# Kernel optimization log

Hardware: AMD Instinct MI355X
Metric: run time of the kernel (lower is better)

The kernel has to match this reference:

```python
import jax, jax.numpy as jnp
import numpy as np

N, E = 50000, 800000
DIM_IN, DIM_H, DIM_OUT, HEADS = 128, 32, 16, 4
HID = DIM_H * HEADS  # 128
FINAL = DIM_OUT * HEADS  # 64
NEG_SLOPE = 0.2


def _glorot(key, shape):
    fan_in, fan_out = shape[0], shape[-1] if len(shape) > 1 else shape[0]
    lim = jnp.sqrt(6.0 / (fan_in + fan_out)).astype(jnp.float32)
    return jax.random.uniform(key, shape, jnp.float32, -lim, lim)


def setup_inputs() -> dict:
    key = jax.random.key(0)
    ks = jax.random.split(key, 16)
    x = jax.random.normal(ks[0], (N, DIM_IN), jnp.float32)
    edge_index = jax.random.randint(ks[1], (2, E), 0, N, dtype=jnp.int64)
    inp = {"x": x, "edge_index": edge_index}
    # layer 1: DIM_IN -> HEADS*DIM_H
    inp["Wl1"] = _glorot(ks[2], (DIM_IN, HEADS * DIM_H))
    inp["Wr1"] = _glorot(ks[3], (DIM_IN, HEADS * DIM_H))
    inp["att1"] = _glorot(ks[4], (HEADS, DIM_H))
    inp["b1"] = jnp.zeros((HEADS * DIM_H,), jnp.float32)
    # layer 2: HID -> HEADS*DIM_H
    inp["Wl2"] = _glorot(ks[5], (HID, HEADS * DIM_H))
    inp["Wr2"] = _glorot(ks[6], (HID, HEADS * DIM_H))
    inp["att2"] = _glorot(ks[7], (HEADS, DIM_H))
    inp["b2"] = jnp.zeros((HEADS * DIM_H,), jnp.float32)
    # layer 3: HID -> HEADS*DIM_OUT
    inp["Wl3"] = _glorot(ks[8], (HID, HEADS * DIM_OUT))
    inp["Wr3"] = _glorot(ks[9], (HID, HEADS * DIM_OUT))
    inp["att3"] = _glorot(ks[10], (HEADS, DIM_OUT))
    inp["b3"] = jnp.zeros((HEADS * DIM_OUT,), jnp.float32)
    return inp


def gatv2_conv(x, src, dst, Wl, Wr, att, b, heads, ch):
    n = x.shape[0]
    xl = (x @ Wl).reshape(n, heads, ch)  # source-side transform
    xr = (x @ Wr).reshape(n, heads, ch)  # target-side transform
    m = xl[src] + xr[dst]                 # [E, H, C]
    e = jnp.einsum('ehc,hc->eh', jax.nn.leaky_relu(m, NEG_SLOPE), att)
    # segment softmax over incoming edges of each dst node
    emax = jax.ops.segment_max(e, dst, num_segments=n)
    ex = jnp.exp(e - emax[dst])
    denom = jax.ops.segment_sum(ex, dst, num_segments=n)
    alpha = ex / denom[dst]               # [E, H]
    out = jax.ops.segment_sum(alpha[:, :, None] * xl[src], dst, num_segments=n)
    return out.reshape(n, heads * ch) + b


def reference(x, edge_index, Wl1, Wr1, att1, b1, Wl2, Wr2, att2, b2, Wl3, Wr3, att3, b3):
    n = x.shape[0]
    loops = jnp.arange(n, dtype=edge_index.dtype)
    src = jnp.concatenate([edge_index[0], loops])  # PyG add_self_loops=True
    dst = jnp.concatenate([edge_index[1], loops])
    # dropout is identity in eval mode
    h = jax.nn.elu(gatv2_conv(x, src, dst, Wl1, Wr1, att1, b1, HEADS, DIM_H))
    h = jax.nn.elu(gatv2_conv(h, src, dst, Wl2, Wr2, att2, b2, HEADS, DIM_H))
    h = gatv2_conv(h, src, dst, Wl3, Wr3, att3, b3, HEADS, DIM_OUT)
    return jax.nn.log_softmax(h, axis=1)
```

## Files before the change

### kernel.cpp

```cpp
#include <hip/hip_runtime.h>
#include <math.h>

constexpr int DIN  = 128;
constexpr int FSH  = 10;
constexpr int NFBM = 64;
constexpr int LCAP = 160;
constexpr int RND  = 4096;
constexpr int FCAP = 18432;

typedef __attribute__((ext_vector_type(8))) short short8;
typedef __attribute__((ext_vector_type(4))) float f32x4;
typedef __attribute__((ext_vector_type(2))) float f32x2;

__device__ __forceinline__ unsigned short f2bf(float f) {
  unsigned u = __float_as_uint(f);
  u = (u + 0x7FFF + ((u >> 16) & 1)) >> 16;
  return (unsigned short)u;
}
__device__ __forceinline__ float bflo(unsigned u) { return __uint_as_float(u << 16); }
__device__ __forceinline__ float bfhi(unsigned u) { return __uint_as_float(u & 0xFFFF0000u); }
__device__ __forceinline__ f32x2 bfpair(unsigned u) {
  f32x2 r; r.x = bflo(u); r.y = bfhi(u); return r;
}
__device__ __forceinline__ f32x2 fabs2(f32x2 v) {
  f32x2 r; r.x = fabsf(v.x); r.y = fabsf(v.y); return r;
}

typedef const __attribute__((address_space(1))) unsigned int guint_t;
typedef __attribute__((address_space(3))) unsigned int luint_t;
__device__ __forceinline__ void async16(const void* g, void* l) {
  __builtin_amdgcn_global_load_lds((guint_t*)g, (luint_t*)l, 16, 0, 0);
}

__device__ __forceinline__ float score8(uint4 u, const f32x2* xrp,
                                        const f32x2* a6, const f32x2* a4, f32x2* xp) {
  xp[0] = bfpair(u.x); xp[1] = bfpair(u.y);
  xp[2] = bfpair(u.z); xp[3] = bfpair(u.w);
  f32x2 acc = {0.f, 0.f};
#pragma unroll
  for (int j = 0; j < 4; ++j) {
    f32x2 t = xp[j] + xrp[j];
    acc += t * a6[j] + fabs2(t) * a4[j];
  }
  float p = acc.x + acc.y;
  p += __shfl_xor(p, 1, 64);
  p += __shfl_xor(p, 2, 64);
  return p;
}

__device__ __forceinline__ float score4(uint2 u, const f32x2* xrp,
                                        const f32x2* a6, const f32x2* a4, f32x2* xp) {
  xp[0] = bfpair(u.x); xp[1] = bfpair(u.y);
  f32x2 acc = {0.f, 0.f};
#pragma unroll
  for (int j = 0; j < 2; ++j) {
    f32x2 t = xp[j] + xrp[j];
    acc += t * a6[j] + fabs2(t) * a4[j];
  }
  float p = acc.x + acc.y;
  p += __shfl_xor(p, 1, 64);
  p += __shfl_xor(p, 2, 64);
  return p;
}


__global__ __launch_bounds__(256) void bucket_append_kernel(const int* __restrict__ ei,
    int* __restrict__ gcnt, unsigned* __restrict__ gpairs, int E, int nfb) {
  __shared__ unsigned buf[NFBM * LCAP];
  __shared__ int cnt[NFBM];
  __shared__ int gbase[NFBM];
  const int tid = threadIdx.x;
  if (tid < NFBM) cnt[tid] = 0;
  __syncthreads();

  const int k0 = blockIdx.x * RND;
  for (int i = tid; i < RND; i += 256) {
    int k = k0 + i;
    if (k >= E) break;
    int src = ei[k], dst = ei[E + k];
    int fb = dst >> FSH;
    int pos = atomicAdd(&cnt[fb], 1);
    if (pos < LCAP)
      buf[fb * LCAP + pos] = (unsigned)src | ((unsigned)(dst & ((1 << FSH) - 1)) << 16);
  }
  __syncthreads();

  if (tid < nfb) gbase[tid] = atomicAdd(&gcnt[tid], min(cnt[tid], LCAP));
  __syncthreads();

  const int wid = tid >> 6, lane = tid & 63;
  for (int fb = wid; fb < nfb; fb += 4) {
    int c  = min(cnt[fb], LCAP);
    int gb = gbase[fb];
    if (gb >= FCAP) continue;
    c = min(c, FCAP - gb);
    unsigned* dstp = gpairs + (size_t)fb * FCAP + gb;
    const unsigned* srcp = &buf[fb * LCAP];
    for (int i = lane; i < c; i += 64) dstp[i] = srcp[i];
  }
}

__global__ __launch_bounds__(256) void bucket_build_kernel(const unsigned* __restrict__ gpairs,
    const int* __restrict__ gcnt, int* __restrict__ row_ptr,
    unsigned short* __restrict__ edge_src, int n, int nfb) {
  const int b   = blockIdx.x;
  const int tid = threadIdx.x;
  const int lane = tid & 63, wid = tid >> 6;
  __shared__ int hist[1024];
  __shared__ int wsum[4];
  __shared__ int base_s;

  const int d0 = b << FSH;
  const int nvalid = min(1 << FSH, n - d0);

  if (wid == 0) {
    int term = 0;
    if (lane < b)
      term = min(gcnt[lane], FCAP) + min(1 << FSH, n - (lane << FSH));
#pragma unroll
    for (int o = 32; o >= 1; o >>= 1) term += __shfl_xor(term, o, 64);
    if (lane == 0) base_s = term;
  }
  for (int i = tid; i < 1024; i += 256) hist[i] = (i < nvalid) ? 1 : 0;
  __syncthreads();

  const int cnt = min(gcnt[b], FCAP);
  const unsigned* bp = gpairs + (size_t)b * FCAP;
  for (int i = tid; i < cnt; i += 256)
    atomicAdd(&hist[bp[i] >> 16], 1);
  __syncthreads();

  const int i4 = tid * 4;
  int h0 = hist[i4], h1 = hist[i4 + 1], h2 = hist[i4 + 2], h3 = hist[i4 + 3];
  int s = h0 + h1 + h2 + h3;
  int incl = s;
#pragma unroll
  for (int o = 1; o < 64; o <<= 1) {
    int t = __shfl_up(incl, o, 64);
    if (lane >= o) incl += t;
  }
  if (lane == 63) wsum[wid] = incl;
  __syncthreads();
  int wo = 0;
  for (int wq = 0; wq < wid; ++wq) wo += wsum[wq];
  const int base = base_s;
  int ex[4];
  ex[0] = wo + incl - s;
  ex[1] = ex[0] + h0;
  ex[2] = ex[1] + h1;
  ex[3] = ex[2] + h2;
#pragma unroll
  for (int j = 0; j < 4; ++j) {
    int d = i4 + j;
    if (d < nvalid) {
      row_ptr[d0 + d] = base + ex[j];
      edge_src[base + ex[j]] = (unsigned short)(d0 + d);
      hist[d] = ex[j] + 1;
    } else if (d0 + d == n) {
      row_ptr[n] = base + ex[j];
    }
  }
  if (b == nfb - 1 && d0 + 1024 <= n && tid == 0) row_ptr[n] = base + cnt + nvalid;
  __syncthreads();

  for (int i = tid; i < cnt; i += 256) {
    unsigned p = bp[i];
    int pos = atomicAdd(&hist[p >> 16], 1);
    edge_src[base + pos] = (unsigned short)(p & 0xFFFFu);
  }
}

__global__ __launch_bounds__(256) void cvt_w_kernel(
    const float* __restrict__ Wl1, const float* __restrict__ Wr1,
    const float* __restrict__ Wl2, const float* __restrict__ Wr2,
    const float* __restrict__ Wl3, const float* __restrict__ Wr3,
    unsigned short* __restrict__ Wt, int* __restrict__ gcnt) {
  if (blockIdx.x == 0 && threadIdx.x < NFBM) gcnt[threadIdx.x] = 0;
  int e = blockIdx.x * 256 + threadIdx.x;
  if (e >= 81920) return;
  const float* src; int N; int off;
  if (e < 65536) {
    int m = e >> 14; off = e & 16383; N = 128;
    src = (m == 0) ? Wl1 : (m == 1) ? Wr1 : (m == 2) ? Wl2 : Wr2;
  } else {
    int e2 = e - 65536; int m = e2 >> 13; off = e2 & 8191; N = 64;
    src = m ? Wr3 : Wl3;
  }
  int nn = off >> 7, k = off & 127;
  Wt[e] = f2bf(src[(size_t)k * N + nn]);
}


template<int NC, bool CVT>
__global__ __launch_bounds__(256) void gemm2_mfma(const void* __restrict__ Ap,
    const unsigned short* __restrict__ Wlt, const unsigned short* __restrict__ Wrt,
    unsigned short* __restrict__ outl, unsigned short* __restrict__ outr, int M) {
  constexpr int WNB = NC / 16;
  __shared__ char lds[16384 + NC * 256];
  char* As = lds;
  char* Ws = lds + 16384;
  const int tid  = threadIdx.x;
  const int w    = tid >> 6, lane = tid & 63;
  const int q    = lane >> 4, r15 = lane & 15;
  const int row0 = blockIdx.x * 64;

  if constexpr (CVT) {
    const float* Af = (const float*)Ap;
    for (int idx = tid * 4; idx < 64 * 128; idx += 1024) {
      int rl = idx >> 7, k = idx & 127;
      int rg = row0 + rl; if (rg >= M) rg = M - 1;
      float4 v = *(const float4*)&Af[(size_t)rg * 128 + k];
      uint2 pk;
      pk.x = (unsigned)f2bf(v.x) | ((unsigned)f2bf(v.y) << 16);
      pk.y = (unsigned)f2bf(v.z) | ((unsigned)f2bf(v.w) << 16);
      char* addr = As + (rl >> 4) * 4096 + (k >> 5) * 1024 +
                   ((((k >> 3) & 3) * 16) + (rl & 15)) * 16 + (k & 7) * 2;
      *(uint2*)addr = pk;
    }
  } else {
    const unsigned short* A = (const unsigned short*)Ap;
    int r = row0 + w * 16 + r15; if (r >= M) r = M - 1;
    const char* g = (const char*)A + (size_t)r * 256 + q * 16;
    char* l = As + w * 4096;
#pragma unroll
    for (int kk = 0; kk < 4; ++kk) async16(g + kk * 64, l + kk * 1024);
  }
  for (int nt = w; nt < WNB; nt += 4) {
    const char* g = (const char*)Wlt + ((size_t)(nt * 16 + r15)) * 256 + q * 16;
    char* l = Ws + nt * 4096;
#pragma unroll
    for (int kk = 0; kk < 4; ++kk) async16(g + kk * 64, l + kk * 1024);
  }
  __syncthreads();

  const char* aw = As + w * 4096;
  f32x4 acc[WNB] = {};
#pragma unroll
  for (int kk = 0; kk < 4; ++kk) {
    short8 af = *(const short8*)(aw + kk * 1024 + (size_t)lane * 16);
#pragma unroll
    for (int nt = 0; nt < WNB; ++nt) {
      short8 bf = *(const short8*)(Ws + (nt * 4 + kk) * 1024 + (size_t)lane * 16);
      acc[nt] = __builtin_amdgcn_mfma_f32_16x16x32_bf16(af, bf, acc[nt], 0, 0, 0);
    }
  }
  {
    int rowb = row0 + w * 16 + q * 4;
#pragma unroll
    for (int nt = 0; nt < WNB; ++nt)
#pragma unroll
      for (int r = 0; r < 4; ++r) {
        int rr = rowb + r;
        if (rr < M) outl[(size_t)rr * NC + nt * 16 + r15] = f2bf(acc[nt][r]);
      }
  }
  __syncthreads();
  for (int nt = w; nt < WNB; nt += 4) {
    const char* g = (const char*)Wrt + ((size_t)(nt * 16 + r15)) * 256 + q * 16;
    char* l = Ws + nt * 4096;
#pragma unroll
    for (int kk = 0; kk < 4; ++kk) async16(g + kk * 64, l + kk * 1024);
  }
  __syncthreads();

  f32x4 acc2[WNB] = {};
#pragma unroll
  for (int kk = 0; kk < 4; ++kk) {
    short8 af = *(const short8*)(aw + kk * 1024 + (size_t)lane * 16);
#pragma unroll
    for (int nt = 0; nt < WNB; ++nt) {
      short8 bf = *(const short8*)(Ws + (nt * 4 + kk) * 1024 + (size_t)lane * 16);
      acc2[nt] = __builtin_amdgcn_mfma_f32_16x16x32_bf16(af, bf, acc2[nt], 0, 0, 0);
    }
  }
  {
    int rowb = row0 + w * 16 + q * 4;
#pragma unroll
    for (int nt = 0; nt < WNB; ++nt)
#pragma unroll
      for (int r = 0; r < 4; ++r) {
        int rr = rowb + r;
        if (rr < M) outr[(size_t)rr * NC + nt * 16 + r15] = f2bf(acc2[nt][r]);
      }
  }
}


__global__ __launch_bounds__(256) void aggregate128_kernel(
    const unsigned short* __restrict__ xl, const unsigned short* __restrict__ xr,
    const float* __restrict__ att, const float* __restrict__ bias,
    const int* __restrict__ row_ptr, const unsigned short* __restrict__ edge_src,
    unsigned short* __restrict__ out, int n) {
  const int tid  = threadIdx.x;
  const int r    = tid & 15;
  const int node = blockIdx.x * 16 + (tid >> 4);
  if (node >= n) return;
  const int c0 = r * 8;

  f32x2 xrp[4];
  {
    uint4 u = *(const uint4*)&xr[(size_t)node * 128 + c0];
    xrp[0] = bfpair(u.x); xrp[1] = bfpair(u.y);
    xrp[2] = bfpair(u.z); xrp[3] = bfpair(u.w);
  }
  f32x2 a6[4], a4[4];
  {
    float4 aa = *(const float4*)&att[c0];
    float4 ab = *(const float4*)&att[c0 + 4];
    float at[8] = {aa.x, aa.y, aa.z, aa.w, ab.x, ab.y, ab.z, ab.w};
#pragma unroll
    for (int j = 0; j < 4; ++j) {
      a6[j].x = 0.6f * at[2 * j];     a6[j].y = 0.6f * at[2 * j + 1];
      a4[j].x = 0.4f * at[2 * j];     a4[j].y = 0.4f * at[2 * j + 1];
    }
  }

  float l = 0.f;
  f32x2 o[4] = {};
  int idx = row_ptr[node];
  const int end = row_ptr[node + 1];

  for (; idx + 4 <= end; idx += 4) {
    int s0 = edge_src[idx],     s1 = edge_src[idx + 1];
    int s2 = edge_src[idx + 2], s3 = edge_src[idx + 3];
    uint4 u0 = *(const uint4*)&xl[(size_t)s0 * 128 + c0];
    uint4 u1 = *(const uint4*)&xl[(size_t)s1 * 128 + c0];
    uint4 u2 = *(const uint4*)&xl[(size_t)s2 * 128 + c0];
    uint4 u3 = *(const uint4*)&xl[(size_t)s3 * 128 + c0];
    f32x2 x0[4], x1[4], x2[4], x3[4];
    float p0 = score8(u0, xrp, a6, a4, x0);
    float p1 = score8(u1, xrp, a6, a4, x1);
    float p2 = score8(u2, xrp, a6, a4, x2);
    float p3 = score8(u3, xrp, a6, a4, x3);
    float e0 = __expf(fminf(p0, 80.f)), e1 = __expf(fminf(p1, 80.f));
    float e2 = __expf(fminf(p2, 80.f)), e3 = __expf(fminf(p3, 80.f));
    l += (e0 + e1) + (e2 + e3);
    f32x2 ev0 = {e0, e0}, ev1 = {e1, e1}, ev2 = {e2, e2}, ev3 = {e3, e3};
#pragma unroll
    for (int j = 0; j < 4; ++j)
      o[j] += ev0 * x0[j] + ev1 * x1[j] + ev2 * x2[j] + ev3 * x3[j];
  }
  for (; idx < end; ++idx) {
    int s0 = edge_src[idx];
    uint4 u0 = *(const uint4*)&xl[(size_t)s0 * 128 + c0];
    f32x2 x0[4];
    float p0 = score8(u0, xrp, a6, a4, x0);
    float e0 = __expf(fminf(p0, 80.f));
    l += e0;
    f32x2 ev0 = {e0, e0};
#pragma unroll
    for (int j = 0; j < 4; ++j) o[j] += ev0 * x0[j];
  }

  float4 b0 = *(const float4*)&bias[c0];
  float4 b1 = *(const float4*)&bias[c0 + 4];
  float bb[8] = {b0.x, b0.y, b0.z, b0.w, b1.x, b1.y, b1.z, b1.w};
  float rl = 1.f / l;
  unsigned short res[8];
#pragma unroll
  for (int j = 0; j < 4; ++j) {
    float v0 = o[j].x * rl + bb[2 * j];
    float v1 = o[j].y * rl + bb[2 * j + 1];
    v0 = v0 > 0.f ? v0 : __expf(v0) - 1.f;
    v1 = v1 > 0.f ? v1 : __expf(v1) - 1.f;
    res[2 * j] = f2bf(v0); res[2 * j + 1] = f2bf(v1);
  }
  uint4 ov;
  ov.x = (unsigned)res[0] | ((unsigned)res[1] << 16);
  ov.y = (unsigned)res[2] | ((unsigned)res[3] << 16);
  ov.z = (unsigned)res[4] | ((unsigned)res[5] << 16);
  ov.w = (unsigned)res[6] | ((unsigned)res[7] << 16);
  *(uint4*)&out[(size_t)node * 128 + c0] = ov;
}


__global__ __launch_bounds__(256) void aggregate64_kernel(
    const unsigned short* __restrict__ xl, const unsigned short* __restrict__ xr,
    const float* __restrict__ att, const float* __restrict__ bias,
    const int* __restrict__ row_ptr, const unsigned short* __restrict__ edge_src,
    float* __restrict__ out, int n) {
  const int tid  = threadIdx.x;
  const int r    = tid & 15;
  const int node = blockIdx.x * 16 + (tid >> 4);
  if (node >= n) return;
  const int c0 = r * 4;

  f32x2 xrp[2];
  {
    uint2 u = *(const uint2*)&xr[(size_t)node * 64 + c0];
    xrp[0] = bfpair(u.x); xrp[1] = bfpair(u.y);
  }
  f32x2 a6[2], a4[2];
  {
    float4 aa = *(const float4*)&att[c0];
    a6[0].x = 0.6f * aa.x; a6[0].y = 0.6f * aa.y;
    a6[1].x = 0.6f * aa.z; a6[1].y = 0.6f * aa.w;
    a4[0].x = 0.4f * aa.x; a4[0].y = 0.4f * aa.y;
    a4[1].x = 0.4f * aa.z; a4[1].y = 0.4f * aa.w;
  }

  float l = 0.f;
  f32x2 o[2] = {};
  int idx = row_ptr[node];
  const int end = row_ptr[node + 1];

  for (; idx + 4 <= end; idx += 4) {
    int s0 = edge_src[idx],     s1 = edge_src[idx + 1];
    int s2 = edge_src[idx + 2], s3 = edge_src[idx + 3];
    uint2 u0 = *(const uint2*)&xl[(size_t)s0 * 64 + c0];
    uint2 u1 = *(const uint2*)&xl[(size_t)s1 * 64 + c0];
    uint2 u2 = *(const uint2*)&xl[(size_t)s2 * 64 + c0];
    uint2 u3 = *(const uint2*)&xl[(size_t)s3 * 64 + c0];
    f32x2 x0[2], x1[2], x2[2], x3[2];
    float p0 = score4(u0, xrp, a6, a4, x0);
    float p1 = score4(u1, xrp, a6, a4, x1);
    float p2 = score4(u2, xrp, a6, a4, x2);
    float p3 = score4(u3, xrp, a6, a4, x3);
    float e0 = __expf(fminf(p0, 80.f)), e1 = __expf(fminf(p1, 80.f));
    float e2 = __expf(fminf(p2, 80.f)), e3 = __expf(fminf(p3, 80.f));
    l += (e0 + e1) + (e2 + e3);
    f32x2 ev0 = {e0, e0}, ev1 = {e1, e1}, ev2 = {e2, e2}, ev3 = {e3, e3};
#pragma unroll
    for (int j = 0; j < 2; ++j)
      o[j] += ev0 * x0[j] + ev1 * x1[j] + ev2 * x2[j] + ev3 * x3[j];
  }
  for (; idx < end; ++idx) {
    int s0 = edge_src[idx];
    uint2 u0 = *(const uint2*)&xl[(size_t)s0 * 64 + c0];
    f32x2 x0[2];
    float p0 = score4(u0, xrp, a6, a4, x0);
    float e0 = __expf(fminf(p0, 80.f));
    l += e0;
    f32x2 ev0 = {e0, e0};
#pragma unroll
    for (int j = 0; j < 2; ++j) o[j] += ev0 * x0[j];
  }

  float4 bv = *(const float4*)&bias[c0];
  float rl = 1.f / l;
  float rr[4];
  rr[0] = o[0].x * rl + bv.x;
  rr[1] = o[0].y * rl + bv.y;
  rr[2] = o[1].x * rl + bv.z;
  rr[3] = o[1].y * rl + bv.w;

  float mx = fmaxf(fmaxf(rr[0], rr[1]), fmaxf(rr[2], rr[3]));
#pragma unroll
  for (int off = 1; off < 16; off <<= 1) mx = fmaxf(mx, __shfl_xor(mx, off, 64));
  float se = __expf(rr[0] - mx) + __expf(rr[1] - mx) +
             __expf(rr[2] - mx) + __expf(rr[3] - mx);
#pragma unroll
  for (int off = 1; off < 16; off <<= 1) se += __shfl_xor(se, off, 64);
  float ls = mx + __logf(se);
  *(float4*)&out[(size_t)node * 64 + c0] =
      make_float4(rr[0] - ls, rr[1] - ls, rr[2] - ls, rr[3] - ls);
}


extern "C" void kernel_launch(void* const* d_in, const int* in_sizes, int n_in,
                              void* d_out, int out_size, void* d_ws, size_t ws_size,
                              hipStream_t stream) {
  const float* x    = (const float*)d_in[0];
  const int*   ei   = (const int*)d_in[1];
  const float* Wl1  = (const float*)d_in[2];
  const float* Wr1  = (const float*)d_in[3];
  const float* att1 = (const float*)d_in[4];
  const float* b1   = (const float*)d_in[5];
  const float* Wl2  = (const float*)d_in[6];
  const float* Wr2  = (const float*)d_in[7];
  const float* att2 = (const float*)d_in[8];
  const float* b2   = (const float*)d_in[9];
  const float* Wl3  = (const float*)d_in[10];
  const float* Wr3  = (const float*)d_in[11];
  const float* att3 = (const float*)d_in[12];
  const float* b3   = (const float*)d_in[13];
  const int n = in_sizes[0] / DIN;
  const int E = in_sizes[1] / 2;
  float* out = (float*)d_out;

  const int nfb = (n + (1 << FSH) - 1) >> FSH;

  unsigned short* xl = (unsigned short*)d_ws;
  unsigned short* xr = xl + (size_t)n * 128;
  unsigned short* h  = xr + (size_t)n * 128;
  unsigned short* Wt = h + (size_t)n * 128;
  unsigned short* Wl1t = Wt, *Wr1t = Wt + 16384;
  unsigned short* Wl2t = Wt + 32768, *Wr2t = Wt + 49152;
  unsigned short* Wl3t = Wt + 65536, *Wr3t = Wt + 73728;
  int* row_ptr  = (int*)(Wt + 81920);
  int* gcnt     = row_ptr + (n + 16);
  unsigned short* edge_src = (unsigned short*)(gcnt + NFBM);
  unsigned* gpairs = (unsigned*)((char*)edge_src +
      ((((size_t)(E + n) * 2) + 15) & ~(size_t)15));

  cvt_w_kernel<<<320, 256, 0, stream>>>(Wl1, Wr1, Wl2, Wr2, Wl3, Wr3, Wt, gcnt);

  bucket_append_kernel<<<(E + RND - 1) / RND, 256, 0, stream>>>(ei, gcnt, gpairs, E, nfb);
  bucket_build_kernel<<<nfb, 256, 0, stream>>>(gpairs, gcnt, row_ptr, edge_src, n, nfb);

  const int gb = (n + 63) / 64;
  const int ab = (n + 15) / 16;

  gemm2_mfma<128, true><<<gb, 256, 0, stream>>>(x, Wl1t, Wr1t, xl, xr, n);
  aggregate128_kernel<<<ab, 256, 0, stream>>>(xl, xr, att1, b1, row_ptr, edge_src, h, n);
  gemm2_mfma<128, false><<<gb, 256, 0, stream>>>(h, Wl2t, Wr2t, xl, xr, n);
  aggregate128_kernel<<<ab, 256, 0, stream>>>(xl, xr, att2, b2, row_ptr, edge_src, h, n);
  gemm2_mfma<64, false><<<gb, 256, 0, stream>>>(h, Wl3t, Wr3t, xl, xr, n);
  aggregate64_kernel<<<ab, 256, 0, stream>>>(xl, xr, att3, b3, row_ptr, edge_src, out, n);
}
```

Before: 311.5 us.

## Accumulate xl+xr sums and subtract xr once; batch 8 edge gathers per iteration

The aggregation kernels now accumulate e*(xl+xr) instead of e*xl, reusing the sum already formed for scoring, and subtract xr once at the end. This relies on the softmax weights summing to one and removes the separate conversion and multiply of the raw xl values. The edge loop also issues all 8 gathered row loads before any compute, to keep more memory requests in flight. The cost is more live registers, which may lower occupancy, plus a small change in float rounding.

Measured after the change: 314.1 us. Within noise of the previous version (+0.8%).

```diff
diff --git a/kernel.cpp b/kernel.cpp
--- a/kernel.cpp
+++ b/kernel.cpp
@@ -32,15 +32,17 @@
   __builtin_amdgcn_global_load_lds((guint_t*)g, (luint_t*)l, 16, 0, 0);
 }
 
-__device__ __forceinline__ float score8(uint4 u, const f32x2* xrp,
-                                        const f32x2* a6, const f32x2* a4, f32x2* xp) {
-  xp[0] = bfpair(u.x); xp[1] = bfpair(u.y);
-  xp[2] = bfpair(u.z); xp[3] = bfpair(u.w);
+__device__ __forceinline__ float scoret8(uint4 u, const f32x2* xrp,
+                                         const f32x2* a, f32x2* t) {
+  t[0] = bfpair(u.x) + xrp[0];
+  t[1] = bfpair(u.y) + xrp[1];
+  t[2] = bfpair(u.z) + xrp[2];
+  t[3] = bfpair(u.w) + xrp[3];
   f32x2 acc = {0.f, 0.f};
 #pragma unroll
   for (int j = 0; j < 4; ++j) {
-    f32x2 t = xp[j] + xrp[j];
-    acc += t * a6[j] + fabs2(t) * a4[j];
+    f32x2 w = t[j] * 0.6f + fabs2(t[j]) * 0.4f;
+    acc += w * a[j];
   }
   float p = acc.x + acc.y;
   p += __shfl_xor(p, 1, 64);
@@ -48,14 +50,15 @@
   return p;
 }
 
-__device__ __forceinline__ float score4(uint2 u, const f32x2* xrp,
-                                        const f32x2* a6, const f32x2* a4, f32x2* xp) {
-  xp[0] = bfpair(u.x); xp[1] = bfpair(u.y);
+__device__ __forceinline__ float scoret4(uint2 u, const f32x2* xrp,
+                                         const f32x2* a, f32x2* t) {
+  t[0] = bfpair(u.x) + xrp[0];
+  t[1] = bfpair(u.y) + xrp[1];
   f32x2 acc = {0.f, 0.f};
 #pragma unroll
   for (int j = 0; j < 2; ++j) {
-    f32x2 t = xp[j] + xrp[j];
-    acc += t * a6[j] + fabs2(t) * a4[j];
+    f32x2 w = t[j] * 0.6f + fabs2(t[j]) * 0.4f;
+    acc += w * a[j];
   }
   float p = acc.x + acc.y;
   p += __shfl_xor(p, 1, 64);
@@ -303,53 +306,47 @@
     xrp[0] = bfpair(u.x); xrp[1] = bfpair(u.y);
     xrp[2] = bfpair(u.z); xrp[3] = bfpair(u.w);
   }
-  f32x2 a6[4], a4[4];
+  f32x2 a[4];
   {
     float4 aa = *(const float4*)&att[c0];
     float4 ab = *(const float4*)&att[c0 + 4];
-    float at[8] = {aa.x, aa.y, aa.z, aa.w, ab.x, ab.y, ab.z, ab.w};
-#pragma unroll
-    for (int j = 0; j < 4; ++j) {
-      a6[j].x = 0.6f * at[2 * j];     a6[j].y = 0.6f * at[2 * j + 1];
-      a4[j].x = 0.4f * at[2 * j];     a4[j].y = 0.4f * at[2 * j + 1];
-    }
+    a[0].x = aa.x; a[0].y = aa.y; a[1].x = aa.z; a[1].y = aa.w;
+    a[2].x = ab.x; a[2].y = ab.y; a[3].x = ab.z; a[3].y = ab.w;
   }
 
   float l = 0.f;
-  f32x2 o[4] = {};
+  f32x2 ot[4] = {};
   int idx = row_ptr[node];
   const int end = row_ptr[node + 1];
 
-  for (; idx + 4 <= end; idx += 4) {
-    int s0 = edge_src[idx],     s1 = edge_src[idx + 1];
-    int s2 = edge_src[idx + 2], s3 = edge_src[idx + 3];
-    uint4 u0 = *(const uint4*)&xl[(size_t)s0 * 128 + c0];
-    uint4 u1 = *(const uint4*)&xl[(size_t)s1 * 128 + c0];
-    uint4 u2 = *(const uint4*)&xl[(size_t)s2 * 128 + c0];
-    uint4 u3 = *(const uint4*)&xl[(size_t)s3 * 128 + c0];
-    f32x2 x0[4], x1[4], x2[4], x3[4];
-    float p0 = score8(u0, xrp, a6, a4, x0);
-    float p1 = score8(u1, xrp, a6, a4, x1);
-    float p2 = score8(u2, xrp, a6, a4, x2);
-    float p3 = score8(u3, xrp, a6, a4, x3);
-    float e0 = __expf(fminf(p0, 80.f)), e1 = __expf(fminf(p1, 80.f));
-    float e2 = __expf(fminf(p2, 80.f)), e3 = __expf(fminf(p3, 80.f));
-    l += (e0 + e1) + (e2 + e3);
-    f32x2 ev0 = {e0, e0}, ev1 = {e1, e1}, ev2 = {e2, e2}, ev3 = {e3, e3};
-#pragma unroll
-    for (int j = 0; j < 4; ++j)
-      o[j] += ev0 * x0[j] + ev1 * x1[j] + ev2 * x2[j] + ev3 * x3[j];
+  for (; idx + 8 <= end; idx += 8) {
+    uint4 u[8];
+#pragma unroll
+    for (int k = 0; k < 8; ++k) {
+      int s = edge_src[idx + k];
+      u[k] = *(const uint4*)&xl[(size_t)s * 128 + c0];
+    }
+#pragma unroll
+    for (int k = 0; k < 8; ++k) {
+      f32x2 t[4];
+      float p = scoret8(u[k], xrp, a, t);
+      float e = __expf(fminf(p, 80.f));
+      l += e;
+      f32x2 ev = {e, e};
+#pragma unroll
+      for (int j = 0; j < 4; ++j) ot[j] += ev * t[j];
+    }
   }
   for (; idx < end; ++idx) {
-    int s0 = edge_src[idx];
-    uint4 u0 = *(const uint4*)&xl[(size_t)s0 * 128 + c0];
-    f32x2 x0[4];
-    float p0 = score8(u0, xrp, a6, a4, x0);
-    float e0 = __expf(fminf(p0, 80.f));
-    l += e0;
-    f32x2 ev0 = {e0, e0};
-#pragma unroll
-    for (int j = 0; j < 4; ++j) o[j] += ev0 * x0[j];
+    int s = edge_src[idx];
+    uint4 u = *(const uint4*)&xl[(size_t)s * 128 + c0];
+    f32x2 t[4];
+    float p = scoret8(u, xrp, a, t);
+    float e = __expf(fminf(p, 80.f));
+    l += e;
+    f32x2 ev = {e, e};
+#pragma unroll
+    for (int j = 0; j < 4; ++j) ot[j] += ev * t[j];
   }
 
   float4 b0 = *(const float4*)&bias[c0];
@@ -359,8 +356,8 @@
   unsigned short res[8];
 #pragma unroll
   for (int j = 0; j < 4; ++j) {
-    float v0 = o[j].x * rl + bb[2 * j];
-    float v1 = o[j].y * rl + bb[2 * j + 1];
+    float v0 = ot[j].x * rl - xrp[j].x + bb[2 * j];
+    float v1 = ot[j].y * rl - xrp[j].y + bb[2 * j + 1];
     v0 = v0 > 0.f ? v0 : __expf(v0) - 1.f;
     v1 = v1 > 0.f ? v1 : __expf(v1) - 1.f;
     res[2 * j] = f2bf(v0); res[2 * j + 1] = f2bf(v1);
@@ -390,59 +387,54 @@
     uint2 u = *(const uint2*)&xr[(size_t)node * 64 + c0];
     xrp[0] = bfpair(u.x); xrp[1] = bfpair(u.y);
   }
-  f32x2 a6[2], a4[2];
+  f32x2 a[2];
   {
     float4 aa = *(const float4*)&att[c0];
-    a6[0].x = 0.6f * aa.x; a6[0].y = 0.6f * aa.y;
-    a6[1].x = 0.6f * aa.z; a6[1].y = 0.6f * aa.w;
-    a4[0].x = 0.4f * aa.x; a4[0].y = 0.4f * aa.y;
-    a4[1].x = 0.4f * aa.z; a4[1].y = 0.4f * aa.w;
+    a[0].x = aa.x; a[0].y = aa.y; a[1].x = aa.z; a[1].y = aa.w;
   }
 
   float l = 0.f;
-  f32x2 o[2] = {};
+  f32x2 ot[2] = {};
   int idx = row_ptr[node];
   const int end = row_ptr[node + 1];
 
-  for (; idx + 4 <= end; idx += 4) {
-    int s0 = edge_src[idx],     s1 = edge_src[idx + 1];
-    int s2 = edge_src[idx + 2], s3 = edge_src[idx + 3];
-    uint2 u0 = *(const uint2*)&xl[(size_t)s0 * 64 + c0];
-    uint2 u1 = *(const uint2*)&xl[(size_t)s1 * 64 + c0];
-    uint2 u2 = *(const uint2*)&xl[(size_t)s2 * 64 + c0];
-    uint2 u3 = *(const uint2*)&xl[(size_t)s3 * 64 + c0];
-    f32x2 x0[2], x1[2], x2[2], x3[2];
-    float p0 = score4(u0, xrp, a6, a4, x0);
-    float p1 = score4(u1, xrp, a6, a4, x1);
-    float p2 = score4(u2, xrp, a6, a4, x2);
-    float p3 = score4(u3, xrp, a6, a4, x3);
-    float e0 = __expf(fminf(p0, 80.f)), e1 = __expf(fminf(p1, 80.f));
-    float e2 = __expf(fminf(p2, 80.f)), e3 = __expf(fminf(p3, 80.f));
-    l += (e0 + e1) + (e2 + e3);
-    f32x2 ev0 = {e0, e0}, ev1 = {e1, e1}, ev2 = {e2, e2}, ev3 = {e3, e3};
-#pragma unroll
-    for (int j = 0; j < 2; ++j)
-      o[j] += ev0 * x0[j] + ev1 * x1[j] + ev2 * x2[j] + ev3 * x3[j];
+  for (; idx + 8 <= end; idx += 8) {
+    uint2 u[8];
+#pragma unroll
+    for (int k = 0; k < 8; ++k) {
+      int s = edge_src[idx + k];
+      u[k] = *(const uint2*)&xl[(size_t)s * 64 + c0];
+    }
+#pragma unroll
+    for (int k = 0; k < 8; ++k) {
+      f32x2 t[2];
+      float p = scoret4(u[k], xrp, a, t);
+      float e = __expf(fminf(p, 80.f));
+      l += e;
+      f32x2 ev = {e, e};
+#pragma unroll
+      for (int j = 0; j < 2; ++j) ot[j] += ev * t[j];
+    }
   }
   for (; idx < end; ++idx) {
-    int s0 = edge_src[idx];
-    uint2 u0 = *(const uint2*)&xl[(size_t)s0 * 64 + c0];
-    f32x2 x0[2];
-    float p0 = score4(u0, xrp, a6, a4, x0);
-    float e0 = __expf(fminf(p0, 80.f));
-    l += e0;
-    f32x2 ev0 = {e0, e0};
-#pragma unroll
-    for (int j = 0; j < 2; ++j) o[j] += ev0 * x0[j];
+    int s = edge_src[idx];
+    uint2 u = *(const uint2*)&xl[(size_t)s * 64 + c0];
+    f32x2 t[2];
+    float p = scoret4(u, xrp, a, t);
+    float e = __expf(fminf(p, 80.f));
+    l += e;
+    f32x2 ev = {e, e};
+#pragma unroll
+    for (int j = 0; j < 2; ++j) ot[j] += ev * t[j];
   }
 
   float4 bv = *(const float4*)&bias[c0];
   float rl = 1.f / l;
   float rr[4];
-  rr[0] = o[0].x * rl + bv.x;
-  rr[1] = o[0].y * rl + bv.y;
-  rr[2] = o[1].x * rl + bv.z;
-  rr[3] = o[1].y * rl + bv.w;
+  rr[0] = ot[0].x * rl - xrp[0].x + bv.x;
+  rr[1] = ot[0].y * rl - xrp[0].y + bv.y;
+  rr[2] = ot[1].x * rl - xrp[1].x + bv.z;
+  rr[3] = ot[1].y * rl - xrp[1].y + bv.w;
 
   float mx = fmaxf(fmaxf(rr[0], rr[1]), fmaxf(rr[2], rr[3]));
 #pragma unroll
```
